# Kernel optimization log

Hardware: AMD Instinct MI355X
Metric: run time of the kernel (lower is better)

The kernel has to match this reference:

```python
import jax, jax.numpy as jnp
import numpy as np

N_NODES = 32768
N_EDGES = 262144
EMB = 64
NUM_HEADS = 4
FEATURE_FDIM = 9
B_MOL = 2048
MAX_PER_MOL = 32


def setup_inputs() -> dict:
    key = jax.random.key(0)
    ks = list(jax.random.split(key, 32))
    nk = lambda: ks.pop()
    inp = {}
    inp['node_feats'] = jax.random.normal(nk(), (N_NODES, FEATURE_FDIM), jnp.float32)
    inp['feature_dist_graph'] = jax.random.normal(nk(), (N_EDGES, FEATURE_FDIM), jnp.float32)
    inp['rij_dist_pairs'] = jax.random.uniform(nk(), (N_EDGES,), jnp.float32)
    see = jax.random.randint(nk(), (N_EDGES, 2), 1, N_NODES + 1, dtype=jnp.int32)
    inp['start_end_env'] = see
    inp['b_scope'] = see[:, 1]  # destination node per edge (index 0 = pad row, never used)
    inp['scope_update'] = jax.random.randint(nk(), (N_EDGES,), 1, N_NODES + 1, dtype=jnp.int32)
    inp['scope_update_lig'] = jax.random.randint(nk(), (N_EDGES,), 1, N_NODES + 1, dtype=jnp.int32)
    inp['l_scope'] = jax.random.randint(nk(), (B_MOL, MAX_PER_MOL), 0, N_NODES + 1, dtype=jnp.int32)
    s = 0.1
    inp['W_emb'] = jax.random.normal(nk(), (FEATURE_FDIM, EMB), jnp.float32) * s
    inp['b_emb'] = jnp.zeros((EMB,), jnp.float32)
    inp['W_dist'] = jax.random.normal(nk(), (FEATURE_FDIM + 1, EMB), jnp.float32) * s
    inp['b_dist'] = jnp.zeros((EMB,), jnp.float32)
    for i in range(NUM_HEADS - 1):
        d = EMB * (i + 1)
        inp[f'fc_W{i}'] = jax.random.normal(nk(), (d, d), jnp.float32) * (1.0 / np.sqrt(d))
        inp[f'fc_b{i}'] = jnp.zeros((d,), jnp.float32)
        inp[f'attn_a{i}'] = jax.random.normal(nk(), (2 * EMB + d, 1), jnp.float32) * s
    return inp


def _segment_attend(logits, vals, seg, num_seg):
    # segment-wise softmax over edges, then weighted scatter-sum to nodes
    m = jax.ops.segment_max(logits, seg, num_segments=num_seg)
    ex = jnp.exp(logits - m[seg])
    den = jax.ops.segment_sum(ex, seg, num_segments=num_seg)
    alpha = ex / den[seg]
    return jax.ops.segment_sum(alpha[:, None] * vals, seg, num_segments=num_seg)


def _forward(node_feats, feature_dist_graph, rij_dist_pairs,
             start_end_env, b_scope, scope_update, scope_update_lig, l_scope,
             W_emb, b_emb, W_dist, b_dist, fc_Ws, fc_bs, attn_as):
    h_orig = node_feats @ W_emb + b_emb                       # [N, EMB]
    h_orig = jnp.concatenate([jnp.zeros((1, EMB), h_orig.dtype), h_orig], axis=0)  # pad row 0
    msg_in = jnp.concatenate([feature_dist_graph, rij_dist_pairs[:, None]], axis=1)
    message = msg_in @ W_dist + b_dist                        # [E, EMB]
    num_seg = h_orig.shape[0]
    tf_feats = h_orig
    for i in range(NUM_HEADS - 1):
        nbr = h_orig[start_end_env]                           # gather: [E, 2, EMB]
        h = message @ fc_Ws[i] + fc_bs[i]                     # [E, D_i]
        logits = jax.nn.leaky_relu(
            jnp.concatenate([nbr[:, 0], nbr[:, 1], h], axis=1) @ attn_as[i],
            negative_slope=0.2)[:, 0]                         # [E]
        out = jax.nn.elu(_segment_attend(logits, h, b_scope, num_seg))  # [N+1, D_i]
        tf_feats = jnp.concatenate([out, h_orig], axis=1)     # merge='cat' -> D_i + EMB
        # updateConnectedDict: rebuild per-edge messages from updated node features
        message = 0.5 * (tf_feats[scope_update_lig] + tf_feats[scope_update])
    cmp_enc = tf_feats[l_scope]                               # [B, P, NUM_HEADS*EMB]
    return cmp_enc.sum(axis=1)                                # [B, NUM_HEADS*EMB]


def reference(node_feats, feature_dist_graph, rij_dist_pairs,
              start_end_env, b_scope, scope_update, scope_update_lig, l_scope,
              W_emb, b_emb, W_dist, b_dist,
              fc_W0, fc_b0, attn_a0, fc_W1, fc_b1, attn_a1, fc_W2, fc_b2, attn_a2):
    return _forward(node_feats, feature_dist_graph, rij_dist_pairs,
                    start_end_env, b_scope, scope_update, scope_update_lig, l_scope,
                    W_emb, b_emb, W_dist, b_dist,
                    [fc_W0, fc_W1, fc_W2], [fc_b0, fc_b1, fc_b2],
                    [attn_a0, attn_a1, attn_a2])
```

## Files before the change

kernel.cpp:

```cpp
#include <hip/hip_runtime.h>
#include <cstdint>
#include <cstddef>

#define NSEG 32769
#define NNODES 32768
#define NE 262144
#define PSZ ((size_t)NSEG * 64)

using f4 = float4;
typedef __attribute__((ext_vector_type(8))) short bf16x8;
typedef __attribute__((ext_vector_type(4))) float f32x4;

__device__ ushort g_tfp[4 * PSZ];
__device__ uint   g_pkA[PSZ];
__device__ uint   g_pk01[PSZ];
__device__ ushort g_msumh[(size_t)NSEG * 192];
__device__ float  g_q[NSEG];
__device__ float  g_p0[3][NSEG];
__device__ float  g_p1[3][NSEG];
__device__ float  g_w2[3][256];
__device__ float  g_wq10[10];
__device__ float  g_cq;
__device__ float  g_wc[640];
__device__ float  g_bcc[64];
__device__ ushort g_wbB[16384];
__device__ ushort g_wbC[36864];
__device__ f4     g_rec[(size_t)NE * 4];
__device__ int    g_counts[NSEG];
__device__ int    g_excl[NSEG];
__device__ int    g_bsum[1024];
__device__ int    g_rowptr[NSEG + 1];
__device__ int    g_cur[NSEG];
__device__ int    g_csr[NE];
__device__ int    g_g1s[NE];
__device__ int    g_g2s[NE];
__device__ float  g_pe1[NE];
__device__ float  g_pe2[NE];
__device__ int    g_bc[128];
__device__ int    g_bcur[128];
__device__ int    g_sorder[NSEG];

#define WREDUCE(x) { x += __shfl_xor(x, 32); x += __shfl_xor(x, 16); \
                     x += __shfl_xor(x, 8);  x += __shfl_xor(x, 4);  \
                     x += __shfl_xor(x, 2);  x += __shfl_xor(x, 1); }
#define WREDMAX(x) { x = fmaxf(x, __shfl_xor(x, 32)); x = fmaxf(x, __shfl_xor(x, 16)); \
                     x = fmaxf(x, __shfl_xor(x, 8));  x = fmaxf(x, __shfl_xor(x, 4));  \
                     x = fmaxf(x, __shfl_xor(x, 2));  x = fmaxf(x, __shfl_xor(x, 1)); }

__device__ __forceinline__ ushort f2bf(float x) {
    uint u = __float_as_uint(x);
    u += 0x7FFF + ((u >> 16) & 1);
    return (ushort)(u >> 16);
}
__device__ __forceinline__ float bfs(ushort u) { return __uint_as_float(((uint)u) << 16); }
__device__ __forceinline__ float bflo(uint u) { return __uint_as_float(u << 16); }
__device__ __forceinline__ float bfhi(uint u) { return __uint_as_float(u & 0xFFFF0000u); }

__global__ __launch_bounds__(256) void k_front(
    const float* __restrict__ node_feats, const float* __restrict__ We,
    const float* __restrict__ be,
    const float* __restrict__ a0, const float* __restrict__ a1, const float* __restrict__ a2,
    const float* __restrict__ W0, const float* __restrict__ W1, const float* __restrict__ W2,
    const float* __restrict__ b0, const float* __restrict__ b1, const float* __restrict__ b2,
    const float* __restrict__ Wd, const float* __restrict__ bd,
    const int* __restrict__ bscope) {
    int tid = threadIdx.x;
    if (blockIdx.x < 513) {
        __shared__ float Ws[576];
        __shared__ float As6[6][68];
        __shared__ float fsAll[576];
        __shared__ float hsAll[64][68];
        int r0 = blockIdx.x * 64;
        for (int i = tid; i < 576; i += 256) Ws[i] = We[i];
        for (int t = tid; t < 384; t += 256) {
            int vec = t >> 6, j = t & 63;
            const float* Av = (vec >> 1) == 0 ? a0 : ((vec >> 1) == 1 ? a1 : a2);
            As6[vec][j] = Av[((vec & 1) << 6) + j];
        }
        for (int t = tid; t < 576; t += 256) {
            int row = r0 + t / 9;
            float v = 0.f;
            if (row >= 1 && row <= NNODES) v = node_feats[(size_t)(row - 1) * 9 + (t % 9)];
            fsAll[t] = v;
        }
        __syncthreads();
        int j = tid & 63;
        float bj = be[j];
#pragma unroll 4
        for (int p = 0; p < 16; p++) {
            int lr = p * 4 + (tid >> 6);
            int row = r0 + lr;
            float acc = bj;
#pragma unroll
            for (int k = 0; k < 9; k++) acc += fsAll[lr * 9 + k] * Ws[k * 64 + j];
            float v = (row == 0 || row >= NSEG) ? 0.f : acc;
            if (row < NSEG) g_tfp[3 * PSZ + (size_t)row * 64 + j] = f2bf(v);
            hsAll[lr][j] = v;
        }
        __syncthreads();
#pragma unroll
        for (int i = 0; i < 12; i++) {
            int task = i * 256 + tid;
            int d = task >> 3, g = tid & 7;
            int lr = d / 6, vec = d % 6;
            float s = 0.f;
#pragma unroll
            for (int jj = 0; jj < 8; jj++)
                s += hsAll[lr][g * 8 + jj] * As6[vec][g * 8 + jj];
            s += __shfl_xor(s, 1); s += __shfl_xor(s, 2); s += __shfl_xor(s, 4);
            int prow = r0 + lr;
            if (g == 0 && prow < NSEG) {
                int iv = vec >> 1;
                if ((vec & 1) == 0) g_p0[iv][prow] = s;
                else                g_p1[iv][prow] = s;
            }
        }
    } else if (blockIdx.x < 518) {
        int pb = blockIdx.x - 513;
        int k = tid;
        if (pb < 3) {
            int it = pb;
            const float* W = it == 0 ? W0 : (it == 1 ? W1 : W2);
            const float* a = it == 0 ? a0 : (it == 1 ? a1 : a2);
            const float* bias = it == 0 ? b0 : (it == 1 ? b1 : b2);
            int d = 64 * (it + 1);
            if (k < d) {
                float s = 0.f;
                for (int jj = 0; jj < d; jj++) s += W[(size_t)k * d + jj] * a[128 + jj];
                g_w2[it][k] = s;
            } else if (k == 255) {
                float c = 0.f;
                for (int jj = 0; jj < d; jj++) c += a[128 + jj] * bias[jj];
                g_w2[it][255] = c;
            }
        } else if (pb == 3) {
            __shared__ float w2s[64];
            if (k < 64) {
                float s = 0.f;
                for (int jj = 0; jj < 64; jj++) s += W0[(size_t)k * 64 + jj] * a0[128 + jj];
                w2s[k] = s;
            }
            __syncthreads();
            if (k < 10) {
                float s = 0.f;
                for (int jj = 0; jj < 64; jj++) s += Wd[(size_t)k * 64 + jj] * w2s[jj];
                g_wq10[k] = s;
            } else if (k == 64) {
                float s = 0.f, c = 0.f;
                for (int jj = 0; jj < 64; jj++) { s += bd[jj] * w2s[jj]; c += a0[128 + jj] * b0[jj]; }
                g_cq = s + c;
            }
        } else {
            for (int t = k; t < 640; t += 256) {
                int kk = t >> 6, jj = t & 63;
                float s = 0.f;
                for (int m = 0; m < 64; m++) s += Wd[kk * 64 + m] * W0[(size_t)m * 64 + jj];
                g_wc[t] = s;
            }
            if (k < 64) {
                float s = b0[k];
                for (int m = 0; m < 64; m++) s += bd[m] * W0[(size_t)m * 64 + k];
                g_bcc[k] = s;
            }
        }
    } else if (blockIdx.x == 518) {
        for (int t = tid; t < 2048; t += 256) {
            int nt = t >> 8, ks = (t >> 6) & 3, l = t & 63;
            int n = nt * 16 + (l & 15);
            int kb = ks * 32 + ((l >> 4) << 3);
            ushort* dst = &g_wbB[(size_t)t * 8];
#pragma unroll
            for (int i = 0; i < 8; i++)
                dst[i] = f2bf(W1[(size_t)(kb + i) * 128 + n]);
        }
    } else if (blockIdx.x <= 520) {
        int half = blockIdx.x - 519;
        for (int t = tid; t < 2304; t += 256) {
            int nt = half * 6 + t / 384;
            int rem = t % 384;
            int ks = rem >> 6, l = rem & 63;
            int n = nt * 16 + (l & 15);
            int kb = ks * 32 + ((l >> 4) << 3);
            ushort* dst = &g_wbC[((size_t)(nt * 6 + ks) * 64 + l) * 8];
#pragma unroll
            for (int i = 0; i < 8; i++)
                dst[i] = f2bf(W2[(size_t)(kb + i) * 192 + n]);
        }
    } else {
        int e = (blockIdx.x - 521) * 256 + tid;
        if (e < NE) atomicAdd(&g_counts[bscope[e]], 1);
    }
}

__global__ void k_scan1() {
    __shared__ int s[256];
    int t = threadIdx.x, i = blockIdx.x * 256 + t;
    int v = (i < NSEG) ? g_counts[i] : 0;
    s[t] = v; __syncthreads();
    for (int off = 1; off < 256; off <<= 1) {
        int tmp = (t >= off) ? s[t - off] : 0;
        __syncthreads();
        s[t] += tmp;
        __syncthreads();
    }
    if (i < NSEG) g_excl[i] = s[t] - v;
    if (t == 255) g_bsum[blockIdx.x] = s[255];
}

__global__ void k_scan2(int nb) {
    __shared__ int s[256];
    int t = threadIdx.x;
    int v = (t < nb) ? g_bsum[t] : 0;
    s[t] = v; __syncthreads();
    for (int off = 1; off < 256; off <<= 1) {
        int tmp = (t >= off) ? s[t - off] : 0;
        __syncthreads();
        s[t] += tmp;
        __syncthreads();
    }
    if (t < nb) g_bsum[t] = s[t] - v;
}

__global__ void k_scan3() {
    __shared__ int lh[128];
    int t = threadIdx.x;
    if (t < 128) lh[t] = 0;
    __syncthreads();
    int i = blockIdx.x * 256 + t;
    if (i < NSEG) {
        g_rowptr[i] = g_excl[i] + g_bsum[i >> 8];
        int cnt = g_counts[i];
        atomicAdd(&lh[cnt > 127 ? 127 : cnt], 1);
    }
    if (i == NSEG) g_rowptr[NSEG] = NE;
    __syncthreads();
    if (t < 128 && lh[t]) atomicAdd(&g_bc[t], lh[t]);
}

__global__ __launch_bounds__(256) void k_scatter(const int* __restrict__ bs,
                                                 const float* __restrict__ fdg,
                                                 const float* __restrict__ rij,
                                                 const int* __restrict__ see,
                                                 const int* __restrict__ g1,
                                                 const int* __restrict__ g2) {
    __shared__ float wqs[10];
    if (threadIdx.x < 10) wqs[threadIdx.x] = g_wq10[threadIdx.x];
    __syncthreads();
    int e = blockIdx.x * 256 + threadIdx.x;
    if (e >= NE) return;
    int seg = bs[e];
    int pos = g_rowptr[seg] + atomicAdd(&g_cur[seg], 1);
    g_csr[pos] = e;
    float x[10];
#pragma unroll
    for (int k = 0; k < 9; k++) x[k] = fdg[(size_t)e * 9 + k];
    x[9] = rij[e];
    int s0 = see[2 * (size_t)e], s1 = see[2 * (size_t)e + 1];
    float q = g_cq;
#pragma unroll
    for (int k = 0; k < 10; k++) q += x[k] * wqs[k];
    float lb0 = q + g_p0[0][s0] + g_p1[0][s1];
    float pe1 = g_p0[1][s0] + g_p1[1][s1];
    float pe2 = g_p0[2][s0] + g_p1[2][s1];
    size_t rb = (size_t)e * 4;
    g_rec[rb + 0] = make_float4(x[0], x[1], x[2], x[3]);
    g_rec[rb + 1] = make_float4(x[4], x[5], x[6], x[7]);
    g_rec[rb + 2] = make_float4(x[8], x[9], lb0, 0.f);
    g_rec[rb + 3] = make_float4(pe1, pe2, __int_as_float(g1[e]), __int_as_float(g2[e]));
}

__global__ __launch_bounds__(256) void k_mid() {
    int tid = threadIdx.x;
    if (blockIdx.x < 129) {
        __shared__ int sc[128];
        __shared__ int lh[128];
        __shared__ int lbase[128];
        if (tid < 128) { sc[tid] = g_bc[tid]; lh[tid] = 0; }
        __syncthreads();
        for (int off = 1; off < 128; off <<= 1) {
            int tmp = (tid >= off && tid < 128) ? sc[tid - off] : 0;
            __syncthreads();
            if (tid < 128) sc[tid] += tmp;
            __syncthreads();
        }
        int seg = blockIdx.x * 256 + tid;
        int bin = 0, lpos = 0;
        bool valid = seg < NSEG;
        if (valid) {
            int cnt = g_rowptr[seg + 1] - g_rowptr[seg];
            bin = cnt > 127 ? 127 : cnt;
            lpos = atomicAdd(&lh[bin], 1);
        }
        __syncthreads();
        if (tid < 128 && lh[tid] > 0)
            lbase[tid] = atomicAdd(&g_bcur[tid], lh[tid]);
        __syncthreads();
        if (valid) {
            int bstart = sc[bin] - g_bc[bin];
            g_sorder[bstart + lbase[bin] + lpos] = seg;
            g_counts[seg] = 0;
            g_cur[seg] = 0;
        }
    } else if (blockIdx.x < 1153) {
        int pos = (blockIdx.x - 129) * 256 + tid;
        if (pos >= NE) return;
        int e = g_csr[pos];
        f4 d = g_rec[(size_t)e * 4 + 3];
        g_pe1[pos] = d.x;
        g_pe2[pos] = d.y;
        g_g1s[pos] = __float_as_int(d.z);
        g_g2s[pos] = __float_as_int(d.w);
    } else {
        __shared__ float Wcs[640];
        __shared__ float bcs[64];
        for (int i = tid; i < 640; i += 256) Wcs[i] = g_wc[i];
        if (tid < 64) bcs[tid] = g_bcc[tid];
        __syncthreads();
        int lane = tid & 63;
        int seg = (blockIdx.x - 1153) * 4 + (tid >> 6);
        if (seg >= NSEG) return;
        int beg = g_rowptr[seg], end = g_rowptr[seg + 1];
        int cnt = end - beg;
        float y[10];
#pragma unroll
        for (int k = 0; k < 10; k++) y[k] = 0.f;

        if (cnt > 0 && cnt <= 64) {
            float l = -1e30f;
            float x[10];
#pragma unroll
            for (int k = 0; k < 10; k++) x[k] = 0.f;
            if (lane < cnt) {
                int e = g_csr[beg + lane];
                size_t rb = (size_t)e * 4;
                f4 r0 = g_rec[rb + 0];
                f4 r1 = g_rec[rb + 1];
                f4 r2 = g_rec[rb + 2];
                x[0] = r0.x; x[1] = r0.y; x[2] = r0.z; x[3] = r0.w;
                x[4] = r1.x; x[5] = r1.y; x[6] = r1.z; x[7] = r1.w;
                x[8] = r2.x; x[9] = r2.y;
                l = r2.z;
                l = l > 0.f ? l : 0.2f * l;
            }
            float m = l;
            WREDMAX(m);
            float ex = (lane < cnt) ? __expf(l - m) : 0.f;
            float den = ex;
            WREDUCE(den);
            float w = ex / den;
#pragma unroll
            for (int k = 0; k < 10; k++) {
                float s = w * x[k];
                WREDUCE(s);
                y[k] = s;
            }
        } else if (cnt > 64) {
            float m = -1e30f;
            for (int t = beg + lane; t < end; t += 64) {
                int e = g_csr[t];
                float l = g_rec[(size_t)e * 4 + 2].z;
                l = l > 0.f ? l : 0.2f * l;
                m = fmaxf(m, l);
            }
            WREDMAX(m);
            float den = 0.f;
            for (int t = beg + lane; t < end; t += 64) {
                int e = g_csr[t];
                float l = g_rec[(size_t)e * 4 + 2].z;
                l = l > 0.f ? l : 0.2f * l;
                den += __expf(l - m);
            }
            WREDUCE(den);
            float rden = 1.f / den;
            float part[10];
#pragma unroll
            for (int k = 0; k < 10; k++) part[k] = 0.f;
            for (int t = beg + lane; t < end; t += 64) {
                int e = g_csr[t];
                size_t rb = (size_t)e * 4;
                f4 r0 = g_rec[rb + 0];
                f4 r1 = g_rec[rb + 1];
                f4 r2 = g_rec[rb + 2];
                float l = r2.z;
                l = l > 0.f ? l : 0.2f * l;
                float w = __expf(l - m) * rden;
                part[0] += w * r0.x; part[1] += w * r0.y; part[2] += w * r0.z; part[3] += w * r0.w;
                part[4] += w * r1.x; part[5] += w * r1.y; part[6] += w * r1.z; part[7] += w * r1.w;
                part[8] += w * r2.x; part[9] += w * r2.y;
            }
#pragma unroll
            for (int k = 0; k < 10; k++) {
                WREDUCE(part[k]);
                y[k] = part[k];
            }
        }
        float o = bcs[lane];
#pragma unroll
        for (int k = 0; k < 10; k++) o += y[k] * Wcs[k * 64 + lane];
        if (cnt == 0) o = 0.f;
        o = o > 0.f ? o : (__expf(o) - 1.f);
        ushort h = g_tfp[3 * PSZ + (size_t)seg * 64 + lane];
        g_pkA[(size_t)seg * 64 + lane] = (uint)f2bf(o) | ((uint)h << 16);
        float qp = o * g_w2[1][lane] + bfs(h) * g_w2[1][64 + lane];
        WREDUCE(qp);
        if (lane == 0) g_q[seg] = qp + g_w2[1][255];
    }
}

template <int NCM>
__global__ __launch_bounds__(256) void k_attendG() {
    const float* __restrict__ pe = (NCM == 2) ? g_pe1 : g_pe2;
    int lane = threadIdx.x & 63;
    int sidx = blockIdx.x * 4 + (threadIdx.x >> 6);
    if (sidx >= NSEG) return;
    int seg = g_sorder[sidx];
    int beg = g_rowptr[seg], end = g_rowptr[seg + 1];
    int cnt = end - beg;
    float acc[NCM];
#pragma unroll
    for (int c = 0; c < NCM; c++) acc[c] = 0.f;

    if (cnt > 0 && cnt <= 64) {
        float l = -1e30f;
        int i1 = 0, i2 = 0;
        if (lane < cnt) {
            i1 = g_g1s[beg + lane]; i2 = g_g2s[beg + lane];
            l = 0.5f * (g_q[i1] + g_q[i2]) + pe[beg + lane];
            l = l > 0.f ? l : 0.2f * l;
        }
        float m = l;
        WREDMAX(m);
        float ex = (lane < cnt) ? __expf(l - m) : 0.f;
        float den = ex;
        WREDUCE(den);
        float w = ex / den;
        for (int t0 = 0; t0 < cnt; t0 += 8) {
            float wt[8]; int a1[8], a2[8];
#pragma unroll
            for (int u = 0; u < 8; u++) {
                int su = t0 + u; su = su > 63 ? 63 : su;
                wt[u] = __shfl(w, su);
                a1[u] = __shfl(i1, su);
                a2[u] = __shfl(i2, su);
            }
            if (NCM == 2) {
                uint ua[8], ub[8];
#pragma unroll
                for (int u = 0; u < 8; u++) {
                    ua[u] = g_pkA[(size_t)a1[u] * 64 + lane];
                    ub[u] = g_pkA[(size_t)a2[u] * 64 + lane];
                }
#pragma unroll
                for (int u = 0; u < 8; u++) {
                    float wh = 0.5f * wt[u];
                    acc[0] += wh * (bflo(ua[u]) + bflo(ub[u]));
                    acc[1] += wh * (bfhi(ua[u]) + bfhi(ub[u]));
                }
            } else {
                uint ua[8], ub[8];
                ushort ha[8], hb[8];
#pragma unroll
                for (int u = 0; u < 8; u++) {
                    size_t b1 = (size_t)a1[u] * 64 + lane, b2 = (size_t)a2[u] * 64 + lane;
                    ua[u] = g_pk01[b1]; ub[u] = g_pk01[b2];
                    ha[u] = g_tfp[3 * PSZ + b1]; hb[u] = g_tfp[3 * PSZ + b2];
                }
#pragma unroll
                for (int u = 0; u < 8; u++) {
                    float wh = 0.5f * wt[u];
                    acc[0] += wh * (bflo(ua[u]) + bflo(ub[u]));
                    acc[1] += wh * (bfhi(ua[u]) + bfhi(ub[u]));
                    acc[2] += wh * (bfs(ha[u]) + bfs(hb[u]));
                }
            }
        }
    } else if (cnt > 64) {
        float m = -1e30f;
        for (int t = beg + lane; t < end; t += 64) {
            float l = 0.5f * (g_q[g_g1s[t]] + g_q[g_g2s[t]]) + pe[t];
            l = l > 0.f ? l : 0.2f * l;
            m = fmaxf(m, l);
        }
        WREDMAX(m);
        float den = 0.f;
        for (int t = beg + lane; t < end; t += 64) {
            float l = 0.5f * (g_q[g_g1s[t]] + g_q[g_g2s[t]]) + pe[t];
            l = l > 0.f ? l : 0.2f * l;
            den += __expf(l - m);
        }
        WREDUCE(den);
        float rden = 1.f / den;
        for (int t = beg; t < end; t++) {
            float l = 0.5f * (g_q[g_g1s[t]] + g_q[g_g2s[t]]) + pe[t];
            l = l > 0.f ? l : 0.2f * l;
            float w = __expf(l - m) * rden;
            float wh = 0.5f * w;
            size_t b1 = (size_t)g_g1s[t] * 64 + lane, b2 = (size_t)g_g2s[t] * 64 + lane;
            if (NCM == 3) {
                uint ua = g_pk01[b1], ub = g_pk01[b2];
                acc[0] += wh * (bflo(ua) + bflo(ub));
                acc[1] += wh * (bfhi(ua) + bfhi(ub));
                acc[2] += wh * (bfs(g_tfp[3 * PSZ + b1]) + bfs(g_tfp[3 * PSZ + b2]));
            } else {
                uint ua = g_pkA[b1], ub = g_pkA[b2];
                acc[0] += wh * (bflo(ua) + bflo(ub));
                acc[1] += wh * (bfhi(ua) + bfhi(ub));
            }
        }
    }
#pragma unroll
    for (int c = 0; c < NCM; c++)
        g_msumh[(size_t)seg * 192 + lane + 64 * c] = f2bf(acc[c]);
}

__global__ __launch_bounds__(256) void k_gemmB(const float* __restrict__ bias) {
    int tid = threadIdx.x;
    if (blockIdx.x == 0 && tid < 128) { g_bc[tid] = 0; g_bcur[tid] = 0; }
    int w = tid >> 6, l = tid & 63;
    int lm = l & 15, lk = l >> 4;
    int r0 = blockIdx.x * 64 + w * 16;
    int arow = r0 + lm;
    size_t abase = (size_t)(arow < NSEG ? arow : 0) * 192;
    f32x4 acc[8];
#pragma unroll
    for (int nt = 0; nt < 8; nt++) acc[nt] = (f32x4){0.f, 0.f, 0.f, 0.f};
#pragma unroll
    for (int ks = 0; ks < 4; ks++) {
        bf16x8 af = *(const bf16x8*)&g_msumh[abase + ks * 32 + lk * 8];
#pragma unroll
        for (int nt = 0; nt < 8; nt++) {
            bf16x8 bf = *(const bf16x8*)&g_wbB[((size_t)(nt * 4 + ks) * 64 + l) * 8];
            acc[nt] = __builtin_amdgcn_mfma_f32_16x16x32_bf16(af, bf, acc[nt], 0, 0, 0);
        }
    }
#pragma unroll
    for (int j = 0; j < 4; j++) {
        int row = r0 + lk * 4 + j;
        bool valid = row < NSEG;
        int rr = valid ? row : 0;
        bool nonempty = valid && (g_rowptr[row + 1] > g_rowptr[row]);
        float qp = 0.f;
#pragma unroll
        for (int nt = 0; nt < 4; nt++) {
            int c = nt * 16 + lm;
            float vl = acc[nt][j] + bias[c];
            float vh = acc[nt + 4][j] + bias[64 + c];
            if (!nonempty) { vl = 0.f; vh = 0.f; }
            vl = vl > 0.f ? vl : (__expf(vl) - 1.f);
            vh = vh > 0.f ? vh : (__expf(vh) - 1.f);
            float hc = bfs(g_tfp[3 * PSZ + (size_t)rr * 64 + c]);
            if (valid) g_pk01[(size_t)row * 64 + c] = (uint)f2bf(vl) | ((uint)f2bf(vh) << 16);
            qp += vl * g_w2[2][c] + vh * g_w2[2][64 + c] + hc * g_w2[2][128 + c];
        }
        qp += __shfl_xor(qp, 1); qp += __shfl_xor(qp, 2);
        qp += __shfl_xor(qp, 4); qp += __shfl_xor(qp, 8);
        if (valid && lm == 0) g_q[row] = qp + g_w2[2][255];
    }
}

__global__ __launch_bounds__(256) void k_gemmC(const float* __restrict__ bias) {
    int tid = threadIdx.x;
    int w = tid >> 6, l = tid & 63;
    int lm = l & 15, lk = l >> 4;
    int r0 = blockIdx.x * 64 + w * 16;
    int arow = r0 + lm;
    size_t abase = (size_t)(arow < NSEG ? arow : 0) * 192;
    f32x4 acc[12];
#pragma unroll
    for (int nt = 0; nt < 12; nt++) acc[nt] = (f32x4){0.f, 0.f, 0.f, 0.f};
#pragma unroll
    for (int ks = 0; ks < 6; ks++) {
        bf16x8 af = *(const bf16x8*)&g_msumh[abase + ks * 32 + lk * 8];
#pragma unroll
        for (int nt = 0; nt < 12; nt++) {
            bf16x8 bf = *(const bf16x8*)&g_wbC[((size_t)(nt * 6 + ks) * 64 + l) * 8];
            acc[nt] = __builtin_amdgcn_mfma_f32_16x16x32_bf16(af, bf, acc[nt], 0, 0, 0);
        }
    }
#pragma unroll
    for (int j = 0; j < 4; j++) {
        int row = r0 + lk * 4 + j;
        if (row >= NSEG) continue;
        bool nonempty = g_rowptr[row + 1] > g_rowptr[row];
#pragma unroll
        for (int nt = 0; nt < 12; nt++) {
            int col = nt * 16 + lm;
            float v = acc[nt][j] + bias[col];
            if (!nonempty) v = 0.f;
            v = v > 0.f ? v : (__expf(v) - 1.f);
            int plane = nt >> 2, c = col & 63;
            g_tfp[(size_t)plane * PSZ + (size_t)row * 64 + c] = f2bf(v);
        }
    }
}

__global__ void k_final(const int* __restrict__ lscope, float* __restrict__ out) {
    __shared__ int idx[32];
    __shared__ float sm[4][256];
    int m = blockIdx.x, tid = threadIdx.x, w = tid >> 6, lane = tid & 63;
    if (tid < 32) idx[tid] = lscope[m * 32 + tid];
    __syncthreads();
    float a0 = 0.f, a1 = 0.f, a2 = 0.f, a3 = 0.f;
#pragma unroll
    for (int j = w * 8; j < w * 8 + 8; j++) {
        size_t base = (size_t)idx[j] * 64 + lane;
        a0 += bfs(g_tfp[base]);
        a1 += bfs(g_tfp[PSZ + base]);
        a2 += bfs(g_tfp[2 * PSZ + base]);
        a3 += bfs(g_tfp[3 * PSZ + base]);
    }
    sm[w][lane] = a0; sm[w][64 + lane] = a1; sm[w][128 + lane] = a2; sm[w][192 + lane] = a3;
    __syncthreads();
    out[(size_t)m * 256 + tid] = sm[0][tid] + sm[1][tid] + sm[2][tid] + sm[3][tid];
}

extern "C" void kernel_launch(void* const* d_in, const int* in_sizes, int n_in,
                              void* d_out, int out_size, void* d_ws, size_t ws_size,
                              hipStream_t stream) {
    const float* node_feats = (const float*)d_in[0];
    const float* fdg        = (const float*)d_in[1];
    const float* rij        = (const float*)d_in[2];
    const int*   see        = (const int*)d_in[3];
    const int*   b_scope    = (const int*)d_in[4];
    const int*   scope_up   = (const int*)d_in[5];
    const int*   scope_lig  = (const int*)d_in[6];
    const int*   l_scope    = (const int*)d_in[7];
    const float* W_emb      = (const float*)d_in[8];
    const float* b_emb      = (const float*)d_in[9];
    const float* W_dist     = (const float*)d_in[10];
    const float* b_dist     = (const float*)d_in[11];
    const float* fc_W[3]   = {(const float*)d_in[12], (const float*)d_in[15], (const float*)d_in[18]};
    const float* fc_b[3]   = {(const float*)d_in[13], (const float*)d_in[16], (const float*)d_in[19]};
    const float* attn_a[3] = {(const float*)d_in[14], (const float*)d_in[17], (const float*)d_in[20]};

    k_front<<<1545, 256, 0, stream>>>(node_feats, W_emb, b_emb,
                                      attn_a[0], attn_a[1], attn_a[2],
                                      fc_W[0], fc_W[1], fc_W[2],
                                      fc_b[0], fc_b[1], fc_b[2],
                                      W_dist, b_dist, b_scope);
    k_scan1<<<129, 256, 0, stream>>>();
    k_scan2<<<1, 256, 0, stream>>>(129);
    k_scan3<<<129, 256, 0, stream>>>();
    k_scatter<<<NE / 256, 256, 0, stream>>>(b_scope, fdg, rij, see, scope_lig, scope_up);
    k_mid<<<9346, 256, 0, stream>>>();

    k_attendG<2><<<8193, 256, 0, stream>>>();
    k_gemmB<<<513, 256, 0, stream>>>(fc_b[1]);
    k_attendG<3><<<8193, 256, 0, stream>>>();
    k_gemmC<<<513, 256, 0, stream>>>(fc_b[2]);

    k_final<<<2048, 256, 0, stream>>>(l_scope, (float*)d_out);
}
```

Baseline: 203.8 us.

## Pack four segments per wavefront in attend kernels with 16-lane groups

```diff
diff --git a/kernel.cpp b/kernel.cpp
--- a/kernel.cpp
+++ b/kernel.cpp
@@ -46,6 +46,10 @@
 #define WREDMAX(x) { x = fmaxf(x, __shfl_xor(x, 32)); x = fmaxf(x, __shfl_xor(x, 16)); \
                      x = fmaxf(x, __shfl_xor(x, 8));  x = fmaxf(x, __shfl_xor(x, 4));  \
                      x = fmaxf(x, __shfl_xor(x, 2));  x = fmaxf(x, __shfl_xor(x, 1)); }
+#define GREDUCE(x) { x += __shfl_xor(x, 8); x += __shfl_xor(x, 4); \
+                     x += __shfl_xor(x, 2); x += __shfl_xor(x, 1); }
+#define GREDMAX(x) { x = fmaxf(x, __shfl_xor(x, 8)); x = fmaxf(x, __shfl_xor(x, 4)); \
+                     x = fmaxf(x, __shfl_xor(x, 2)); x = fmaxf(x, __shfl_xor(x, 1)); }
 
 __device__ __forceinline__ ushort f2bf(float x) {
     uint u = __float_as_uint(x);
@@ -408,12 +412,7 @@
 }
 
 template <int NCM>
-__global__ __launch_bounds__(256) void k_attendG() {
-    const float* __restrict__ pe = (NCM == 2) ? g_pe1 : g_pe2;
-    int lane = threadIdx.x & 63;
-    int sidx = blockIdx.x * 4 + (threadIdx.x >> 6);
-    if (sidx >= NSEG) return;
-    int seg = g_sorder[sidx];
+__device__ __forceinline__ void attend_full(int seg, const float* __restrict__ pe, int lane) {
     int beg = g_rowptr[seg], end = g_rowptr[seg + 1];
     int cnt = end - beg;
     float acc[NCM];
@@ -511,6 +510,115 @@
 #pragma unroll
     for (int c = 0; c < NCM; c++)
         g_msumh[(size_t)seg * 192 + lane + 64 * c] = f2bf(acc[c]);
+}
+
+template <int NCM>
+__global__ __launch_bounds__(256) void k_attendG() {
+    const float* __restrict__ pe = (NCM == 2) ? g_pe1 : g_pe2;
+    int tid = threadIdx.x;
+    int lane = tid & 63;
+    int sidx0 = (blockIdx.x * 4 + (tid >> 6)) * 4;
+    if (sidx0 >= NSEG) return;
+    int g = lane >> 4, ln = lane & 15;
+    int sidx = sidx0 + g;
+    bool gvalid = sidx < NSEG;
+    int seg = gvalid ? g_sorder[sidx] : 0;
+    int beg = gvalid ? g_rowptr[seg] : 0;
+    int end = gvalid ? g_rowptr[seg + 1] : 0;
+    int cnt = end - beg;
+    int mx = cnt;
+    mx = max(mx, __shfl_xor(mx, 16));
+    mx = max(mx, __shfl_xor(mx, 32));
+
+    if (mx <= 16) {
+        float l = -1e30f;
+        int i1 = 0, i2 = 0;
+        if (gvalid && ln < cnt) {
+            i1 = g_g1s[beg + ln]; i2 = g_g2s[beg + ln];
+            l = 0.5f * (g_q[i1] + g_q[i2]) + pe[beg + ln];
+            l = l > 0.f ? l : 0.2f * l;
+        }
+        float m = l;
+        GREDMAX(m);
+        float ex = (gvalid && ln < cnt) ? __expf(l - m) : 0.f;
+        float den = ex;
+        GREDUCE(den);
+        float w = ex / den;
+        float acc[NCM][4];
+#pragma unroll
+        for (int c = 0; c < NCM; c++)
+#pragma unroll
+            for (int j = 0; j < 4; j++) acc[c][j] = 0.f;
+        int gbase = lane & 48;
+        for (int t0 = 0; t0 < cnt; t0 += 4) {
+            float wt[4]; int a1[4], a2[4];
+#pragma unroll
+            for (int u = 0; u < 4; u++) {
+                int su = t0 + u; su = su > 15 ? 15 : su;
+                wt[u] = __shfl(w, gbase + su);
+                a1[u] = __shfl(i1, gbase + su);
+                a2[u] = __shfl(i2, gbase + su);
+            }
+            if (NCM == 2) {
+                uint4 pa[4], pb[4];
+#pragma unroll
+                for (int u = 0; u < 4; u++) {
+                    pa[u] = *(const uint4*)&g_pkA[(size_t)a1[u] * 64 + ln * 4];
+                    pb[u] = *(const uint4*)&g_pkA[(size_t)a2[u] * 64 + ln * 4];
+                }
+#pragma unroll
+                for (int u = 0; u < 4; u++) {
+                    float wh = 0.5f * wt[u];
+                    uint ua[4] = {pa[u].x, pa[u].y, pa[u].z, pa[u].w};
+                    uint ub[4] = {pb[u].x, pb[u].y, pb[u].z, pb[u].w};
+#pragma unroll
+                    for (int j = 0; j < 4; j++) {
+                        acc[0][j] += wh * (bflo(ua[j]) + bflo(ub[j]));
+                        acc[1][j] += wh * (bfhi(ua[j]) + bfhi(ub[j]));
+                    }
+                }
+            } else {
+                uint4 pa[4], pb[4];
+                ushort4 ha[4], hb[4];
+#pragma unroll
+                for (int u = 0; u < 4; u++) {
+                    size_t b1 = (size_t)a1[u] * 64 + ln * 4, b2 = (size_t)a2[u] * 64 + ln * 4;
+                    pa[u] = *(const uint4*)&g_pk01[b1];
+                    pb[u] = *(const uint4*)&g_pk01[b2];
+                    ha[u] = *(const ushort4*)&g_tfp[3 * PSZ + b1];
+                    hb[u] = *(const ushort4*)&g_tfp[3 * PSZ + b2];
+                }
+#pragma unroll
+                for (int u = 0; u < 4; u++) {
+                    float wh = 0.5f * wt[u];
+                    uint ua[4] = {pa[u].x, pa[u].y, pa[u].z, pa[u].w};
+                    uint ub[4] = {pb[u].x, pb[u].y, pb[u].z, pb[u].w};
+                    ushort va[4] = {ha[u].x, ha[u].y, ha[u].z, ha[u].w};
+                    ushort vb[4] = {hb[u].x, hb[u].y, hb[u].z, hb[u].w};
+#pragma unroll
+                    for (int j = 0; j < 4; j++) {
+                        acc[0][j] += wh * (bflo(ua[j]) + bflo(ub[j]));
+                        acc[1][j] += wh * (bfhi(ua[j]) + bfhi(ub[j]));
+                        acc[2][j] += wh * (bfs(va[j]) + bfs(vb[j]));
+                    }
+                }
+            }
+        }
+        if (gvalid) {
+#pragma unroll
+            for (int c = 0; c < NCM; c++) {
+                ushort4 o;
+                o.x = f2bf(acc[c][0]); o.y = f2bf(acc[c][1]);
+                o.z = f2bf(acc[c][2]); o.w = f2bf(acc[c][3]);
+                *(ushort4*)&g_msumh[(size_t)seg * 192 + c * 64 + ln * 4] = o;
+            }
+        }
+    } else {
+        for (int ii = 0; ii < 4; ii++) {
+            int si = sidx0 + ii;
+            if (si < NSEG) attend_full<NCM>(g_sorder[si], pe, lane);
+        }
+    }
 }
 
 __global__ __launch_bounds__(256) void k_gemmB(const float* __restrict__ bias) {
@@ -644,9 +752,9 @@
     k_scatter<<<NE / 256, 256, 0, stream>>>(b_scope, fdg, rij, see, scope_lig, scope_up);
     k_mid<<<9346, 256, 0, stream>>>();
 
-    k_attendG<2><<<8193, 256, 0, stream>>>();
+    k_attendG<2><<<2049, 256, 0, stream>>>();
     k_gemmB<<<513, 256, 0, stream>>>(fc_b[1]);
-    k_attendG<3><<<8193, 256, 0, stream>>>();
+    k_attendG<3><<<2049, 256, 0, stream>>>();
     k_gemmC<<<513, 256, 0, stream>>>(fc_b[2]);
 
     k_final<<<2048, 256, 0, stream>>>(l_scope, (float*)d_out);
```

Result: slower. 215.2 us (+5.6%).
